# Kernel optimization log

Measured on AMD Instinct MI355X. Metric: run time of the kernel, lower is better.

The kernel has to match this reference:

```python
import jax, jax.numpy as jnp
import numpy as np

TOPK_RATIO = 0.2
DICE_WEIGHT = 0.5
SHAPE = (2, 1, 128, 192, 192)


def setup_inputs() -> dict:
    key = jax.random.key(0)
    k1, k2 = jax.random.split(key)
    logits = jax.random.normal(k1, SHAPE, dtype=jnp.float32)
    targets = jax.random.uniform(k2, SHAPE, dtype=jnp.float32)
    return {"logits": logits, "targets": targets}


def _bce_with_logits(x, t):
    # stable: max(x,0) - x*t + log(1+exp(-|x|))
    return jnp.maximum(x, 0.0) - x * t + jnp.log1p(jnp.exp(-jnp.abs(x)))


def reference(logits, targets):
    # --- TopK BCE ---
    flat_loss = _bce_with_logits(logits, targets).reshape(-1)
    n = flat_loss.shape[0]
    k_samples = max(1, int(n * TOPK_RATIO))
    topk_losses, _ = jax.lax.top_k(flat_loss, k_samples)
    bce = jnp.mean(topk_losses)

    # --- Soft Dice ---
    p = jax.nn.sigmoid(logits).reshape(-1)
    t = targets.reshape(-1)
    intersection = jnp.sum(p * t)
    union = jnp.sum(p) + jnp.sum(t)
    dice = (2.0 * intersection + 1e-06) / (union + 1e-06)
    dice_loss = 1.0 - dice

    return bce + DICE_WEIGHT * dice_loss
```

## Files before the change

### kernel.cpp

```cpp
#include <hip/hip_runtime.h>
#include <math.h>
#include <limits.h>

#define NB1 8192
#define NB2 4096
#define VEC 4
#define NREP 4

__device__ unsigned g_H1[NB1];
__device__ unsigned g_hist2[NREP * NB2];
__device__ float    g_band[2];
__device__ unsigned g_done1 = 0;

__device__ __forceinline__ void elem_f(float x, float t, float& l, float& p) {
    float e = __expf(-fabsf(x));
    l = fmaxf(x, 0.f) - x * t + __logf(1.f + e);
    float r = __builtin_amdgcn_rcpf(1.f + e);
    p = (x >= 0.f) ? r : e * r;
}

__global__ __launch_bounds__(256) void sample_band_kernel(
    const float4* __restrict__ x4, const float4* __restrict__ t4,
    int n4, long long ks, long long M)
{
    __shared__ unsigned lh[NB1];
    __shared__ int is_last;
    for (int i = threadIdx.x; i < NB1; i += 256) lh[i] = 0u;
    __syncthreads();

    int nth = gridDim.x * 256;
    int tid = blockIdx.x * 256 + threadIdx.x;
    int S4 = n4 >> 5;
    int i0 = tid, i1 = tid + nth;

    int f40 = ((i0 >> 8) << 13) + (i0 & 255);
    int f41 = ((i1 >> 8) << 13) + (i1 & 255);
    bool v0 = (i0 < S4) && (f40 < n4);
    bool v1 = (i1 < S4) && (f41 < n4);

    float4 xa, ta, xb, tb;
    if (v0) { xa = x4[f40]; ta = t4[f40]; }
    if (v1) { xb = x4[f41]; tb = t4[f41]; }
    if (v0) {
        float xs[4] = {xa.x, xa.y, xa.z, xa.w};
        float ts[4] = {ta.x, ta.y, ta.z, ta.w};
        #pragma unroll
        for (int c = 0; c < 4; ++c) {
            float l, p; elem_f(xs[c], ts[c], l, p);
            atomicAdd(&lh[__float_as_uint(l) >> 19], 1u);
        }
    }
    if (v1) {
        float xs[4] = {xb.x, xb.y, xb.z, xb.w};
        float ts[4] = {tb.x, tb.y, tb.z, tb.w};
        #pragma unroll
        for (int c = 0; c < 4; ++c) {
            float l, p; elem_f(xs[c], ts[c], l, p);
            atomicAdd(&lh[__float_as_uint(l) >> 19], 1u);
        }
    }
    __syncthreads();
    for (int i = threadIdx.x; i < NB1; i += 256) {
        unsigned c = lh[i];
        if (c) atomicAdd(&g_H1[i], c);
    }
    __syncthreads();

    if (threadIdx.x == 0) {
        __threadfence();
        is_last = (atomicAdd(&g_done1, 1u) == (unsigned)(gridDim.x - 1));
    }
    __syncthreads();
    if (!is_last) return;
    __threadfence();

    const uint4* hv = (const uint4*)g_H1;
    uint4* lv = (uint4*)lh;
    for (int i = threadIdx.x; i < NB1 / 4; i += 256) lv[i] = hv[i];
    __syncthreads();
    for (int i = threadIdx.x; i < NB1; i += 256) g_H1[i] = 0u;
    if (threadIdx.x == 0) g_done1 = 0u;

    if (threadIdx.x < 64) {
        int lane = threadIdx.x;
        int base = lane << 7;
        unsigned long long chunk = 0;
        for (int j = 0; j < 128; ++j) chunk += lh[base + j];
        unsigned long long s = chunk;
        #pragma unroll
        for (int off = 1; off < 64; off <<= 1) {
            unsigned long long v = __shfl_down(s, off);
            if (lane + off < 64) s += v;
        }
        unsigned long long above = s - chunk;

        int my_bhi = INT_MAX, my_blo = -1;
        unsigned long long c = above;
        for (int j = 127; j >= 0; --j) {
            unsigned h = lh[base + j];
            if ((long long)(c + h) < ks - M) my_bhi = base + j;
            if ((long long)c > ks + M && my_blo < 0) my_blo = base + j;
            c += h;
        }
        #pragma unroll
        for (int off = 32; off; off >>= 1) {
            int a = __shfl_down(my_bhi, off); my_bhi = min(my_bhi, a);
            int b = __shfl_down(my_blo, off); my_blo = max(my_blo, b);
        }
        if (lane == 0) {
            int bhi = (my_bhi == INT_MAX) ? (NB1 - 1) : my_bhi;
            int blo = my_blo;
            float vhi = __uint_as_float((unsigned)bhi << 19);
            float vlo = (blo < 0) ? 0.f : __uint_as_float((unsigned)(blo + 1) << 19);
            if (!(vlo < vhi)) vlo = 0.f;
            g_band[0] = vlo;
            g_band[1] = vhi;
        }
    }
}

__device__ __forceinline__ void process4(
    float4 xv, float4 tv, float vlo, float vhi, float scale,
    float& sp, float& spt, float& st, float& sgt, unsigned& cnt,
    unsigned (&lhist)[NB2])
{
    float xs[4] = {xv.x, xv.y, xv.z, xv.w};
    float ts[4] = {tv.x, tv.y, tv.z, tv.w};
    #pragma unroll
    for (int c = 0; c < 4; ++c) {
        float l, p;
        elem_f(xs[c], ts[c], l, p);
        sp += p; spt += p * ts[c]; st += ts[c];
        if (l >= vhi) { cnt++; sgt += l; }
        else if (l >= vlo) {
            int b = min((int)((l - vlo) * scale), NB2 - 1);
            atomicAdd(&lhist[b], 1u);
        }
    }
}

__global__ __launch_bounds__(256, 4) void main_kernel(
    const float4* __restrict__ x4, const float4* __restrict__ t4,
    float* __restrict__ q0, float* __restrict__ q1,
    float* __restrict__ q2, float* __restrict__ q3, unsigned* __restrict__ qc,
    const float* __restrict__ xg, const float* __restrict__ tg,
    int n, int n4)
{
    __shared__ unsigned lhist[NB2];
    for (int i = threadIdx.x; i < NB2; i += 256) lhist[i] = 0u;
    __syncthreads();

    float vlo = g_band[0], vhi = g_band[1];
    float scale = (float)NB2 / (vhi - vlo);

    int base = blockIdx.x * (256 * VEC) + threadIdx.x;
    float sp = 0.f, spt = 0.f, st = 0.f, sgt = 0.f;
    unsigned cnt = 0;

    bool full = (blockIdx.x + 1) * (256 * VEC) <= n4;
    if (full) {
        float4 xv[VEC], tv[VEC];
        #pragma unroll
        for (int j = 0; j < VEC; ++j) xv[j] = x4[base + j * 256];
        #pragma unroll
        for (int j = 0; j < VEC; ++j) tv[j] = t4[base + j * 256];
        #pragma unroll
        for (int j = 0; j < VEC; ++j)
            process4(xv[j], tv[j], vlo, vhi, scale, sp, spt, st, sgt, cnt, lhist);
    } else {
        for (int j = 0; j < VEC; ++j) {
            int idx = base + j * 256;
            if (idx < n4)
                process4(x4[idx], t4[idx], vlo, vhi, scale, sp, spt, st, sgt, cnt, lhist);
        }
    }
    int tail0 = n4 << 2;
    if (blockIdx.x == 0 && threadIdx.x < (n - tail0)) {
        float x = xg[tail0 + threadIdx.x], t = tg[tail0 + threadIdx.x];
        float l, p;
        elem_f(x, t, l, p);
        sp += p; spt += p * t; st += t;
        if (l >= vhi) { cnt++; sgt += l; }
        else if (l >= vlo) {
            int b = min((int)((l - vlo) * scale), NB2 - 1);
            atomicAdd(&lhist[b], 1u);
        }
    }

    __syncthreads();
    {
        unsigned* dst = &g_hist2[(blockIdx.x & (NREP - 1)) * NB2];
        for (int i = threadIdx.x; i < NB2; i += 256) {
            unsigned c = lhist[i];
            if (c) atomicAdd(&dst[i], c);
        }
    }

    #pragma unroll
    for (int off = 32; off; off >>= 1) {
        sp  += __shfl_down(sp,  off);
        spt += __shfl_down(spt, off);
        st  += __shfl_down(st,  off);
        sgt += __shfl_down(sgt, off);
        cnt += __shfl_down(cnt, off);
    }
    __shared__ float    rs[4][4];
    __shared__ unsigned rc[4];
    int w = threadIdx.x >> 6;
    if ((threadIdx.x & 63) == 0) {
        rs[w][0] = sp; rs[w][1] = spt; rs[w][2] = st; rs[w][3] = sgt; rc[w] = cnt;
    }
    __syncthreads();
    if (threadIdx.x == 0) {
        float a0 = 0, a1 = 0, a2 = 0, a3 = 0;
        unsigned c = 0;
        #pragma unroll
        for (int i = 0; i < 4; ++i) {
            a0 += rs[i][0]; a1 += rs[i][1]; a2 += rs[i][2]; a3 += rs[i][3]; c += rc[i];
        }
        q0[blockIdx.x] = a0; q1[blockIdx.x] = a1; q2[blockIdx.x] = a2;
        q3[blockIdx.x] = a3; qc[blockIdx.x] = c;
    }
}

__global__ __launch_bounds__(1024) void final_kernel(
    const float* __restrict__ q0, const float* __restrict__ q1,
    const float* __restrict__ q2, const float* __restrict__ q3,
    const unsigned* __restrict__ qc, int nblocks,
    float* __restrict__ out, long long k)
{
    __shared__ unsigned lh[NB2];
    __shared__ double red[16][5];
    __shared__ double fin[5];

    for (int i = threadIdx.x; i < NB2; i += 1024) {
        unsigned s = 0;
        #pragma unroll
        for (int r = 0; r < NREP; ++r) {
            s += g_hist2[r * NB2 + i];
            g_hist2[r * NB2 + i] = 0u;
        }
        lh[i] = s;
    }

    double a0 = 0, a1 = 0, a2 = 0, a3 = 0, a4 = 0;
    for (int i = threadIdx.x; i < nblocks; i += 1024) {
        a0 += (double)q0[i]; a1 += (double)q1[i]; a2 += (double)q2[i];
        a3 += (double)q3[i]; a4 += (double)qc[i];
    }
    #pragma unroll
    for (int off = 32; off; off >>= 1) {
        a0 += __shfl_down(a0, off); a1 += __shfl_down(a1, off);
        a2 += __shfl_down(a2, off); a3 += __shfl_down(a3, off);
        a4 += __shfl_down(a4, off);
    }
    int w = threadIdx.x >> 6;
    if ((threadIdx.x & 63) == 0) {
        red[w][0] = a0; red[w][1] = a1; red[w][2] = a2; red[w][3] = a3; red[w][4] = a4;
    }
    __syncthreads();
    if (threadIdx.x == 0) {
        double f0 = 0, f1 = 0, f2 = 0, f3 = 0, f4 = 0;
        for (int i = 0; i < 16; ++i) {
            f0 += red[i][0]; f1 += red[i][1]; f2 += red[i][2];
            f3 += red[i][3]; f4 += red[i][4];
        }
        fin[0] = f0; fin[1] = f1; fin[2] = f2; fin[3] = f3; fin[4] = f4;
    }
    __syncthreads();
    if (threadIdx.x >= 64) return;

    int lane = threadIdx.x;
    double SP = fin[0], SPT = fin[1], ST = fin[2], SGT = fin[3];
    long long CNT = (long long)fin[4];

    double vlo = (double)g_band[0], vhi = (double)g_band[1];
    double binw = (vhi - vlo) / NB2;
    long long k2 = k - CNT;

    int base = lane << 6;
    unsigned long long cchunk = 0;
    double wchunk = 0.0;
    for (int j = 0; j < 64; ++j) {
        unsigned h = lh[base + j];
        cchunk += h;
        wchunk += (double)h * (vlo + (base + j + 0.5) * binw);
    }
    unsigned long long cs = cchunk;
    double wsum = wchunk;
    #pragma unroll
    for (int off = 1; off < 64; off <<= 1) {
        unsigned long long cv = __shfl_down(cs, off);
        double wv = __shfl_down(wsum, off);
        if (lane + off < 64) { cs += cv; wsum += wv; }
    }
    unsigned long long total = __shfl(cs, 0);
    double wtotal = __shfl(wsum, 0);

    double I = SPT, U = SP + ST;
    double dice_part = 0.5 * (1.0 - (2.0 * I + 1e-6) / (U + 1e-6));

    if (k2 <= 0) {
        if (lane == 0) out[0] = (float)(SGT / (double)k + dice_part);
        return;
    }
    if ((unsigned long long)k2 > total) {
        if (lane == 0) {
            double sum_top = SGT + wtotal + (double)(k2 - (long long)total) * vlo;
            out[0] = (float)(sum_top / (double)k + dice_part);
        }
        return;
    }
    unsigned long long c = cs - cchunk;
    double wacc = wsum - wchunk;
    for (int j = 63; j >= 0; --j) {
        unsigned h = lh[base + j];
        double val = vlo + (base + j + 0.5) * binw;
        if (c < (unsigned long long)k2 && (unsigned long long)k2 <= c + h) {
            double sum_top = SGT + wacc + (double)((long long)k2 - (long long)c) * val;
            out[0] = (float)(sum_top / (double)k + dice_part);
        }
        c += h;
        wacc += (double)h * val;
    }
}

extern "C" void kernel_launch(void* const* d_in, const int* in_sizes, int n_in,
                              void* d_out, int out_size, void* d_ws, size_t ws_size,
                              hipStream_t stream)
{
    const float* x = (const float*)d_in[0];
    const float* t = (const float*)d_in[1];
    float* out = (float*)d_out;
    int n = in_sizes[0];
    int n4 = n >> 2;
    long long k = (long long)((double)n * 0.2);
    if (k < 1) k = 1;

    long long S = (long long)(n4 >> 5) * 4;
    long long ks = (S > 0) ? (long long)((double)k * (double)S / (double)n) : 0;
    long long M = 4096;

    int tilesz = 256 * VEC;
    int grid = (n4 + tilesz - 1) / tilesz;
    if (grid < 1) grid = 1;

    int S4 = n4 >> 5;
    int sgrid = (S4 + 511) / 512;
    if (sgrid < 1) sgrid = 1;

    unsigned char* ws = (unsigned char*)d_ws;
    size_t pstride = (((size_t)grid * 4) + 255) & ~(size_t)255;
    float*    q0 = (float*)(ws);
    float*    q1 = (float*)(ws + pstride);
    float*    q2 = (float*)(ws + 2 * pstride);
    float*    q3 = (float*)(ws + 3 * pstride);
    unsigned* qc = (unsigned*)(ws + 4 * pstride);

    sample_band_kernel<<<sgrid, 256, 0, stream>>>((const float4*)x, (const float4*)t,
                                                  n4, ks, M);
    main_kernel<<<grid, 256, 0, stream>>>((const float4*)x, (const float4*)t,
                                          q0, q1, q2, q3, qc, x, t, n, n4);
    final_kernel<<<1, 1024, 0, stream>>>(q0, q1, q2, q3, qc, grid, out, k);
}
```

Baseline: 150.0 us.

## Use persistent grid with double-buffered tile loads and per-block histogram copies

The main kernel now runs a fixed 768-block grid. Each block walks tiles in a grid-stride loop and prefetches the next tile into a second register buffer while it processes the current one. The global atomic merge of the band histogram is replaced by each block writing its own histogram copy, followed by a separate merge kernel that sums the copies per bin. The sampling kernel also reads only one float4 per thread with a narrower band margin. This adds an extra kernel launch, about 12 MB of histogram writes and reads, and higher register pressure from the double buffering.

```diff
diff --git a/kernel.cpp b/kernel.cpp
--- a/kernel.cpp
+++ b/kernel.cpp
@@ -5,10 +5,10 @@
 #define NB1 8192
 #define NB2 4096
 #define VEC 4
-#define NREP 4
+#define TILE_F4 1024
+#define GRID_MAIN 768
 
 __device__ unsigned g_H1[NB1];
-__device__ unsigned g_hist2[NREP * NB2];
 __device__ float    g_band[2];
 __device__ unsigned g_done1 = 0;
 
@@ -28,31 +28,16 @@
     for (int i = threadIdx.x; i < NB1; i += 256) lh[i] = 0u;
     __syncthreads();
 
-    int nth = gridDim.x * 256;
     int tid = blockIdx.x * 256 + threadIdx.x;
     int S4 = n4 >> 5;
-    int i0 = tid, i1 = tid + nth;
-
-    int f40 = ((i0 >> 8) << 13) + (i0 & 255);
-    int f41 = ((i1 >> 8) << 13) + (i1 & 255);
-    bool v0 = (i0 < S4) && (f40 < n4);
-    bool v1 = (i1 < S4) && (f41 < n4);
-
-    float4 xa, ta, xb, tb;
-    if (v0) { xa = x4[f40]; ta = t4[f40]; }
-    if (v1) { xb = x4[f41]; tb = t4[f41]; }
-    if (v0) {
+
+    int f4 = ((tid >> 8) << 13) + (tid & 255);
+    bool v = (tid < S4) && (f4 < n4);
+
+    if (v) {
+        float4 xa = x4[f4], ta = t4[f4];
         float xs[4] = {xa.x, xa.y, xa.z, xa.w};
         float ts[4] = {ta.x, ta.y, ta.z, ta.w};
-        #pragma unroll
-        for (int c = 0; c < 4; ++c) {
-            float l, p; elem_f(xs[c], ts[c], l, p);
-            atomicAdd(&lh[__float_as_uint(l) >> 19], 1u);
-        }
-    }
-    if (v1) {
-        float xs[4] = {xb.x, xb.y, xb.z, xb.w};
-        float ts[4] = {tb.x, tb.y, tb.z, tb.w};
         #pragma unroll
         for (int c = 0; c < 4; ++c) {
             float l, p; elem_f(xs[c], ts[c], l, p);
@@ -89,8 +74,8 @@
         unsigned long long s = chunk;
         #pragma unroll
         for (int off = 1; off < 64; off <<= 1) {
-            unsigned long long v = __shfl_down(s, off);
-            if (lane + off < 64) s += v;
+            unsigned long long v2 = __shfl_down(s, off);
+            if (lane + off < 64) s += v2;
         }
         unsigned long long above = s - chunk;
 
@@ -119,28 +104,9 @@
     }
 }
 
-__device__ __forceinline__ void process4(
-    float4 xv, float4 tv, float vlo, float vhi, float scale,
-    float& sp, float& spt, float& st, float& sgt, unsigned& cnt,
-    unsigned (&lhist)[NB2])
-{
-    float xs[4] = {xv.x, xv.y, xv.z, xv.w};
-    float ts[4] = {tv.x, tv.y, tv.z, tv.w};
-    #pragma unroll
-    for (int c = 0; c < 4; ++c) {
-        float l, p;
-        elem_f(xs[c], ts[c], l, p);
-        sp += p; spt += p * ts[c]; st += ts[c];
-        if (l >= vhi) { cnt++; sgt += l; }
-        else if (l >= vlo) {
-            int b = min((int)((l - vlo) * scale), NB2 - 1);
-            atomicAdd(&lhist[b], 1u);
-        }
-    }
-}
-
 __global__ __launch_bounds__(256, 4) void main_kernel(
     const float4* __restrict__ x4, const float4* __restrict__ t4,
+    unsigned* __restrict__ hcopies,
     float* __restrict__ q0, float* __restrict__ q1,
     float* __restrict__ q2, float* __restrict__ q3, unsigned* __restrict__ qc,
     const float* __restrict__ xg, const float* __restrict__ tg,
@@ -153,30 +119,89 @@
     float vlo = g_band[0], vhi = g_band[1];
     float scale = (float)NB2 / (vhi - vlo);
 
-    int base = blockIdx.x * (256 * VEC) + threadIdx.x;
+    int tid = threadIdx.x;
+    int ntiles = (n4 + TILE_F4 - 1) / TILE_F4;
+    int fullTiles = n4 / TILE_F4;
+
     float sp = 0.f, spt = 0.f, st = 0.f, sgt = 0.f;
     unsigned cnt = 0;
 
-    bool full = (blockIdx.x + 1) * (256 * VEC) <= n4;
-    if (full) {
-        float4 xv[VEC], tv[VEC];
-        #pragma unroll
-        for (int j = 0; j < VEC; ++j) xv[j] = x4[base + j * 256];
-        #pragma unroll
-        for (int j = 0; j < VEC; ++j) tv[j] = t4[base + j * 256];
-        #pragma unroll
-        for (int j = 0; j < VEC; ++j)
-            process4(xv[j], tv[j], vlo, vhi, scale, sp, spt, st, sgt, cnt, lhist);
-    } else {
+    float4 xA[VEC], tA[VEC], xB[VEC], tB[VEC];
+
+#define LOADT(XD, TD, tile) do { \
+        int _b = (tile) * TILE_F4 + tid; \
+        _Pragma("unroll") \
+        for (int _j = 0; _j < VEC; ++_j) XD[_j] = x4[_b + _j * 256]; \
+        _Pragma("unroll") \
+        for (int _j = 0; _j < VEC; ++_j) TD[_j] = t4[_b + _j * 256]; \
+    } while (0)
+
+#define PROCT(XD, TD) do { \
+        _Pragma("unroll") \
+        for (int _j = 0; _j < VEC; ++_j) { \
+            float _xs[4] = {XD[_j].x, XD[_j].y, XD[_j].z, XD[_j].w}; \
+            float _ts[4] = {TD[_j].x, TD[_j].y, TD[_j].z, TD[_j].w}; \
+            _Pragma("unroll") \
+            for (int _c = 0; _c < 4; ++_c) { \
+                float _l, _p; \
+                elem_f(_xs[_c], _ts[_c], _l, _p); \
+                sp += _p; spt += _p * _ts[_c]; st += _ts[_c]; \
+                if (_l >= vhi) { cnt++; sgt += _l; } \
+                else if (_l >= vlo) { \
+                    int _bn = min((int)((_l - vlo) * scale), NB2 - 1); \
+                    atomicAdd(&lhist[_bn], 1u); \
+                } \
+            } \
+        } \
+    } while (0)
+
+    int t0 = blockIdx.x;
+    if (t0 < fullTiles) {
+        LOADT(xA, tA, t0);
+        int tn = t0 + GRID_MAIN;
+        while (tn < fullTiles) {
+            LOADT(xB, tB, tn);
+            PROCT(xA, tA);
+            tn += GRID_MAIN;
+            if (tn < fullTiles) {
+                LOADT(xA, tA, tn);
+                PROCT(xB, tB);
+                tn += GRID_MAIN;
+            } else {
+                PROCT(xB, tB);
+                goto full_done;
+            }
+        }
+        PROCT(xA, tA);
+full_done: ;
+    }
+
+    if (fullTiles < ntiles && blockIdx.x == (fullTiles % GRID_MAIN)) {
+        int base = fullTiles * TILE_F4 + tid;
         for (int j = 0; j < VEC; ++j) {
             int idx = base + j * 256;
-            if (idx < n4)
-                process4(x4[idx], t4[idx], vlo, vhi, scale, sp, spt, st, sgt, cnt, lhist);
-        }
-    }
+            if (idx < n4) {
+                float4 xv = x4[idx], tv = t4[idx];
+                float xs[4] = {xv.x, xv.y, xv.z, xv.w};
+                float ts[4] = {tv.x, tv.y, tv.z, tv.w};
+                #pragma unroll
+                for (int c = 0; c < 4; ++c) {
+                    float l, p;
+                    elem_f(xs[c], ts[c], l, p);
+                    sp += p; spt += p * ts[c]; st += ts[c];
+                    if (l >= vhi) { cnt++; sgt += l; }
+                    else if (l >= vlo) {
+                        int b = min((int)((l - vlo) * scale), NB2 - 1);
+                        atomicAdd(&lhist[b], 1u);
+                    }
+                }
+            }
+        }
+    }
+
     int tail0 = n4 << 2;
-    if (blockIdx.x == 0 && threadIdx.x < (n - tail0)) {
-        float x = xg[tail0 + threadIdx.x], t = tg[tail0 + threadIdx.x];
+    if (blockIdx.x == 0 && tid < (n - tail0)) {
+        float x = xg[tail0 + tid], t = tg[tail0 + tid];
         float l, p;
         elem_f(x, t, l, p);
         sp += p; spt += p * t; st += t;
@@ -189,11 +214,9 @@
 
     __syncthreads();
     {
-        unsigned* dst = &g_hist2[(blockIdx.x & (NREP - 1)) * NB2];
-        for (int i = threadIdx.x; i < NB2; i += 256) {
-            unsigned c = lhist[i];
-            if (c) atomicAdd(&dst[i], c);
-        }
+        uint4* dst = (uint4*)(hcopies + (size_t)blockIdx.x * NB2);
+        const uint4* src = (const uint4*)lhist;
+        for (int i = tid; i < NB2 / 4; i += 256) dst[i] = src[i];
     }
 
     #pragma unroll
@@ -206,12 +229,12 @@
     }
     __shared__ float    rs[4][4];
     __shared__ unsigned rc[4];
-    int w = threadIdx.x >> 6;
-    if ((threadIdx.x & 63) == 0) {
+    int w = tid >> 6;
+    if ((tid & 63) == 0) {
         rs[w][0] = sp; rs[w][1] = spt; rs[w][2] = st; rs[w][3] = sgt; rc[w] = cnt;
     }
     __syncthreads();
-    if (threadIdx.x == 0) {
+    if (tid == 0) {
         float a0 = 0, a1 = 0, a2 = 0, a3 = 0;
         unsigned c = 0;
         #pragma unroll
@@ -221,9 +244,24 @@
         q0[blockIdx.x] = a0; q1[blockIdx.x] = a1; q2[blockIdx.x] = a2;
         q3[blockIdx.x] = a3; qc[blockIdx.x] = c;
     }
+#undef LOADT
+#undef PROCT
+}
+
+__global__ __launch_bounds__(128) void merge_kernel(
+    const unsigned* __restrict__ hcopies, unsigned* __restrict__ merged,
+    int ncopies)
+{
+    int bin = blockIdx.x * 128 + threadIdx.x;
+    unsigned s = 0;
+    const unsigned* p = hcopies + bin;
+    #pragma unroll 8
+    for (int r = 0; r < ncopies; ++r) s += p[(size_t)r * NB2];
+    merged[bin] = s;
 }
 
 __global__ __launch_bounds__(1024) void final_kernel(
+    const unsigned* __restrict__ merged,
     const float* __restrict__ q0, const float* __restrict__ q1,
     const float* __restrict__ q2, const float* __restrict__ q3,
     const unsigned* __restrict__ qc, int nblocks,
@@ -233,15 +271,7 @@
     __shared__ double red[16][5];
     __shared__ double fin[5];
 
-    for (int i = threadIdx.x; i < NB2; i += 1024) {
-        unsigned s = 0;
-        #pragma unroll
-        for (int r = 0; r < NREP; ++r) {
-            s += g_hist2[r * NB2 + i];
-            g_hist2[r * NB2 + i] = 0u;
-        }
-        lh[i] = s;
-    }
+    for (int i = threadIdx.x; i < NB2; i += 1024) lh[i] = merged[i];
 
     double a0 = 0, a1 = 0, a2 = 0, a3 = 0, a4 = 0;
     for (int i = threadIdx.x; i < nblocks; i += 1024) {
@@ -339,27 +369,30 @@
 
     long long S = (long long)(n4 >> 5) * 4;
     long long ks = (S > 0) ? (long long)((double)k * (double)S / (double)n) : 0;
-    long long M = 4096;
-
-    int tilesz = 256 * VEC;
-    int grid = (n4 + tilesz - 1) / tilesz;
-    if (grid < 1) grid = 1;
+    long long M = 2048;
 
     int S4 = n4 >> 5;
-    int sgrid = (S4 + 511) / 512;
+    int sgrid = (S4 + 255) / 256;
     if (sgrid < 1) sgrid = 1;
 
     unsigned char* ws = (unsigned char*)d_ws;
-    size_t pstride = (((size_t)grid * 4) + 255) & ~(size_t)255;
-    float*    q0 = (float*)(ws);
-    float*    q1 = (float*)(ws + pstride);
-    float*    q2 = (float*)(ws + 2 * pstride);
-    float*    q3 = (float*)(ws + 3 * pstride);
-    unsigned* qc = (unsigned*)(ws + 4 * pstride);
+    unsigned* hcopies = (unsigned*)ws;
+    size_t ho = (size_t)GRID_MAIN * NB2 * sizeof(unsigned);
+    unsigned* merged = (unsigned*)(ws + ho);
+    size_t po = ho + NB2 * sizeof(unsigned);
+    size_t pstride = (((size_t)GRID_MAIN * 4) + 255) & ~(size_t)255;
+    float*    q0 = (float*)(ws + po);
+    float*    q1 = (float*)(ws + po + pstride);
+    float*    q2 = (float*)(ws + po + 2 * pstride);
+    float*    q3 = (float*)(ws + po + 3 * pstride);
+    unsigned* qc = (unsigned*)(ws + po + 4 * pstride);
 
     sample_band_kernel<<<sgrid, 256, 0, stream>>>((const float4*)x, (const float4*)t,
                                                   n4, ks, M);
-    main_kernel<<<grid, 256, 0, stream>>>((const float4*)x, (const float4*)t,
-                                          q0, q1, q2, q3, qc, x, t, n, n4);
-    final_kernel<<<1, 1024, 0, stream>>>(q0, q1, q2, q3, qc, grid, out, k);
-}
+    main_kernel<<<GRID_MAIN, 256, 0, stream>>>((const float4*)x, (const float4*)t,
+                                               hcopies, q0, q1, q2, q3, qc,
+                                               x, t, n, n4);
+    merge_kernel<<<NB2 / 128, 128, 0, stream>>>(hcopies, merged, GRID_MAIN);
+    final_kernel<<<1, 1024, 0, stream>>>(merged, q0, q1, q2, q3, qc,
+                                         GRID_MAIN, out, k);
+}
```

New measurement: 174.5 us. 1.16x slower.
